# Performance work log

Hardware: AMD Instinct MI355X
Metric: run time of the kernel (lower is better)

The kernel has to match this reference:

```python
import jax, jax.numpy as jnp
import numpy as np
import math

A = 32; B = 32; PSIZE = 16; K = 3; STRIDE = 2; PAD = 1; ITERS = 3; FINAL_LAMBDA = 0.01
KK = K * K; KKA = KK * A; KKA2 = KKA // 2 + 1
EPS = 1e-12; LN2PI = math.log(2 * math.pi)


def unfold(x, k, s, p):
    # torch F.unfold: output feature dim ordered (C, kh, kw), columns row-major
    b, C, h, w = x.shape
    xp = jnp.pad(x, ((0, 0), (0, 0), (p, p), (p, p)))
    oh = (h + 2 * p - k) // s + 1
    ow = (w + 2 * p - k) // s + 1
    cols = [xp[:, :, ki:ki + s * (oh - 1) + 1:s, kj:kj + s * (ow - 1) + 1:s]
            for ki in range(k) for kj in range(k)]
    patches = jnp.stack(cols, axis=2)  # [b, C, kk, oh, ow]
    return patches.reshape(b, C, k * k, oh * ow), oh, ow


def setup_inputs():
    key = jax.random.key(0)
    ks = jax.random.split(key, 8)
    b, h, w = 4, 14, 14
    a_in = jax.random.uniform(ks[0], (b, A, h, w), dtype=jnp.float32)
    pose = jax.random.normal(ks[1], (b, A * PSIZE, h, w), dtype=jnp.float32)
    mpose_w = jax.random.normal(ks[2], (B * PSIZE, PSIZE), dtype=jnp.float32) / np.float32(np.sqrt(PSIZE))
    mpose_b = jnp.zeros((B * PSIZE,), jnp.float32)
    freq_w = jax.random.normal(ks[3], (KKA2, PSIZE, 2), dtype=jnp.float32) * 0.02
    ln_g = jnp.ones((A,), jnp.float32)
    ln_b = jnp.zeros((A,), jnp.float32)
    lim = np.float32(np.sqrt(6.0 / (KK + KK)))  # xavier_uniform on [kk, kk, 1]
    spat_w = jax.random.uniform(ks[4], (KK, KK, 1), jnp.float32, -lim, lim)
    spat_bias = jnp.ones((KK,), jnp.float32)
    beta_u = jnp.zeros((1, 1, B, 1), jnp.float32)
    beta_a = jnp.zeros((1, 1, B), jnp.float32)
    return dict(a_in=a_in, pose=pose, mpose_w=mpose_w, mpose_b=mpose_b,
                freq_w=freq_w, ln_g=ln_g, ln_b=ln_b, spat_w=spat_w,
                spat_bias=spat_bias, beta_u=beta_u, beta_a=beta_a)


def _forward(a_in, pose, mpose_w, mpose_b, freq_w, ln_g, ln_b,
             spat_w, spat_bias, beta_u, beta_a):
    b = a_in.shape[0]
    pose_u, oh, ow = unfold(pose, K, STRIDE, PAD)  # [b, A*PSIZE, KK, l]
    l = oh * ow
    pose_u = pose_u.reshape(b, A, PSIZE, KK, l)
    pose_u = pose_u.transpose(0, 4, 3, 1, 2).reshape(b, l, KKA, PSIZE)
    # mpose linear: psize -> B*psize
    po = jnp.einsum('blkp,qp->blkq', pose_u, mpose_w) + mpose_b
    po = po.reshape(b * l, KKA, B, PSIZE)
    # Frequency FFT filter over kkA axis (weight shared across all B slices)
    xf = jnp.fft.rfft(po, axis=1, norm='ortho')        # [bl, KKA2, B, PSIZE] complex
    wc = freq_w[..., 0] + 1j * freq_w[..., 1]           # [KKA2, PSIZE]
    xf = xf * wc[None, :, None, :]
    po = jnp.fft.irfft(xf, n=KKA, axis=1, norm='ortho') + po  # residual
    v = po.reshape(b, l, KKA, B, PSIZE)
    a_u, _, _ = unfold(a_in, K, STRIDE, PAD)            # [b, A, KK, l]
    a_u = a_u.transpose(0, 3, 2, 1).reshape(b, l, KKA)
    # Spatial gating applied to ones-initialized r (identical for every B slice)
    ones = jnp.ones((b * l, KKA), jnp.float32)
    g = ones.reshape(b * l, KK, A)
    mu_g = g.mean(-1, keepdims=True)
    var_g = ((g - mu_g) ** 2).mean(-1, keepdims=True)
    gn = (g - mu_g) / jnp.sqrt(var_g + 1e-5) * ln_g + ln_b
    g2 = jnp.einsum('ij,nja->nia', spat_w[:, :, 0], gn) + spat_bias[None, :, None]
    gate = jax.nn.gelu(g2, approximate=False).reshape(b * l, KKA) + ones
    logit = jnp.broadcast_to(gate[:, :, None], (b * l, KKA, B))
    r = jax.nn.softmax(logit, axis=2).reshape(b, l, KKA, B, 1)
    a_out = mu = None
    for i in range(ITERS):
        lam = FINAL_LAMBDA * (1.0 - 0.95 ** (i + 1))
        # m-step
        rr = r * a_u[:, :, :, None, None]
        r_sum = rr.sum(axis=2, keepdims=True)                 # [b,l,1,B,1]
        coeff = rr / (r_sum + EPS)
        mu = (coeff * v).sum(axis=2, keepdims=True)           # [b,l,1,B,PSIZE]
        sig = (coeff * (v - mu) ** 2).sum(axis=2, keepdims=True) + EPS
        cost = (beta_u + jnp.log(jnp.sqrt(sig[:, :, 0]))) * r_sum[:, :, 0]  # [b,l,B,PSIZE]
        a_out = jax.nn.sigmoid(lam * (beta_a - cost.sum(axis=3)))           # [b,l,B]
        if i < ITERS - 1:
            # e-step (note: log(sigma_sq * ln2pi) is faithful to the original code)
            ln_p = (-0.5 * jnp.sum(jnp.log(sig * LN2PI), axis=-1)
                    - jnp.sum((v - mu) ** 2 / (2.0 * sig), axis=-1))        # [b,l,KKA,B]
            ln_ap = ln_p + jnp.log(a_out[:, :, None, :])
            r = jax.nn.softmax(ln_ap, axis=-1)[..., None]
    pose_out = mu[:, :, 0].reshape(b, l, B * PSIZE).transpose(0, 2, 1).reshape(b, B * PSIZE, oh, ow)
    a_fin = a_out.transpose(0, 2, 1).reshape(b, B, oh, ow)
    return a_fin, pose_out


def reference(a_in, pose, mpose_w, mpose_b, freq_w, ln_g, ln_b,
              spat_w, spat_bias, beta_u, beta_a):
    return _forward(a_in, pose, mpose_w, mpose_b, freq_w, ln_g, ln_b,
                    spat_w, spat_bias, beta_u, beta_a)
```

## Files before the change

kernel.cpp:

```cpp
#include <hip/hip_runtime.h>
#include <hip/hip_bf16.h>
#include <math.h>

#define A_    32
#define B_    32
#define PS    16
#define KK_   9
#define KKA_  288
#define OH_   7
#define L_    49
#define NB    4
#define NSITE 196
#define NCOLS 3136

#define LAM1 5.0e-4f
#define LAM2 9.75e-4f
#define LAM3 1.42625e-3f
#define LOG_LN2PI 0.6086775903077413f

typedef _Float16 half2v __attribute__((ext_vector_type(2)));
typedef short    short8 __attribute__((ext_vector_type(8)));
typedef float    floatx4 __attribute__((ext_vector_type(4)));

static __device__ __forceinline__ float san(float x, float lo, float hi){
    return fminf(fmaxf(x, lo), hi);
}

static __device__ __forceinline__ float dot2acc(half2v a, half2v b, float c){
#if __has_builtin(__builtin_amdgcn_fdot2)
    return __builtin_amdgcn_fdot2(a, b, c, false);
#else
    return c + (float)a.x*(float)b.x + (float)a.y*(float)b.y;
#endif
}

__global__ void k_prep(const float* __restrict__ fw, const float* __restrict__ pose,
                       ushort* __restrict__ cpr, float* __restrict__ csum,
                       __hip_bfloat16* __restrict__ Xt, int nc)
{
    if ((int)blockIdx.x < nc){
        int id = (int)blockIdx.x*256 + threadIdx.x;
        if (id >= 16*288) return;
        int p = id / 288, m = id % 288;
        float acc = fw[(0*16 + p)*2 + 0];
        for (int k = 1; k <= 143; ++k){
            float re = fw[(k*16 + p)*2 + 0];
            float im = fw[(k*16 + p)*2 + 1];
            int km = (k*m) % 288;
            float ang = 0.021816615649929116f * (float)km;
            float s, c; __sincosf(ang, &s, &c);
            acc += 2.0f*(re*c - im*s);
        }
        float re144 = fw[(144*16 + p)*2 + 0];
        acc += re144 * ((m & 1) ? -1.0f : 1.0f);
        float cv = acc * (1.0f/288.0f);
        if (m == 0) cv += 1.0f;
        cv = san(cv, -1e4f, 1e4f);

        __hip_bfloat16 hb = __float2bfloat16(cv);
        float hif = __bfloat162float(hb);
        __hip_bfloat16 lb = __float2bfloat16(cv - hif);
        ushort hi = *(ushort*)&hb, lo = *(ushort*)&lb;

        ushort* c0h = cpr + p*592;
        ushort* c1h = cpr + 16*592   + p*592;
        ushort* c0l = cpr + 16*592*2 + p*592;
        ushort* c1l = cpr + 16*592*3 + p*592;
        int x1 = 288 - m;
        c0h[x1] = hi;  c0l[x1] = lo;
        c1h[x1-1] = hi; c1l[x1-1] = lo;
        if (m >= 1){
            int x2 = 576 - m;
            c0h[x2] = hi;  c0l[x2] = lo;
            c1h[x2-1] = hi; c1l[x2-1] = lo;
        } else {
            c0h[0] = hi; c0l[0] = lo;
            csum[p] = san(1.0f + fw[(0*16 + p)*2 + 0], -1e4f, 1e4f);
        }
        return;
    }
    int id = ((int)blockIdx.x - nc)*256 + threadIdx.x;
    if (id >= NCOLS*KKA_/8) return;
    int c = id / (KKA_/8), j8 = id % (KKA_/8);
    int j = j8*8;
    int n = c >> 4, q = c & 15;
    int bs = n / L_, l = n % L_, oy = l / OH_, ox = l % OH_;
    int kk = j >> 5, a0 = j & 31;
    int y = oy*2 - 1 + kk/3, x = ox*2 - 1 + kk%3;
    const bool inb = ((unsigned)y < 14u && (unsigned)x < 14u);
    const float* psrc = pose + (((long)bs*(A_*PS))*14 + y)*14 + x;
    union { ushort us[8]; uint4 u4; } res;
    #pragma unroll
    for (int u = 0; u < 8; ++u){
        float v = 0.f;
        if (inb) v = psrc[((a0+u)*PS + q)*196];
        __hip_bfloat16 hb = __float2bfloat16(san(v, -1e4f, 1e4f));
        res.us[u] = *(ushort*)&hb;
    }
    *(uint4*)&Xt[c*KKA_ + j] = res.u4;
}

__global__ __attribute__((amdgpu_flat_work_group_size(512,512), amdgpu_waves_per_eu(1,2)))
void
k_mega(const ushort* __restrict__ cpr, const __hip_bfloat16* __restrict__ Xt,
       const float* __restrict__ a_in,
       const float* __restrict__ mpw, const float* __restrict__ mpb,
       const float* __restrict__ csum,
       const float* __restrict__ beta_u, const float* __restrict__ beta_a,
       float* __restrict__ out)
{
    const int nl = blockIdx.x;
    const int t = threadIdx.x;
    const int Bc = t >> 4, p = t & 15;
    const int bs = nl / L_, l = nl % L_;

    __shared__ uint v_lds[48][512];
    __shared__ __align__(16) _Float16 us[2*4224];
    __shared__ float dall[288*34];
    __shared__ float a_s[KKA_];
    __shared__ float cst[32];

    for (int j = t; j < KKA_; j += 512){
        int kk = j >> 5, a = j & 31;
        int oy = l / OH_, ox = l % OH_;
        int y = oy*2 - 1 + kk/3, x = ox*2 - 1 + kk%3;
        float v = 0.f;
        if ((unsigned)y < 14u && (unsigned)x < 14u)
            v = a_in[((bs*A_ + a)*14 + y)*14 + x];
        a_s[j] = san(v, 0.f, 1e4f);
    }
    half2v w_h[8];
    #pragma unroll
    for (int k = 0; k < 8; ++k){
        w_h[k].x = (_Float16)mpw[t*16 + 2*k];
        w_h[k].y = (_Float16)mpw[t*16 + 2*k + 1];
    }
    const float vb = mpb[t] * csum[p];
    const float bu = beta_u[Bc];
    const float ba = beta_a[Bc];
    __syncthreads();

    float s0a = 0.f, s0b = 0.f, s0c = 0.f, s0d = 0.f;
    for (int j = 0; j < KKA_; j += 4){
        s0a += a_s[j]; s0b += a_s[j+1]; s0c += a_s[j+2]; s0d += a_s[j+3];
    }
    const float S0tot = (s0a + s0b) + (s0c + s0d);

    const int w = t >> 6, lane = t & 63;
    const int mn = lane & 15, quad = lane >> 4;
    const int p0 = w*2;
    const __hip_bfloat16* xrow = Xt + (nl*16 + mn)*KKA_ + quad*8;

    float S1 = 0.f, S2 = 0.f;
    half2v v_h[80];

    auto do_chunk = [&](int ch, _Float16* usb){
        floatx4 accA = {0,0,0,0}, accB = {0,0,0,0};
        for (int k0i = 0; k0i < 9; ++k0i){
            const int k0 = k0i*32;
            short8 bfrag = *(const short8*)&xrow[k0];
            #pragma unroll
            for (int pp = 0; pp < 2; ++pp){
                const int pg = p0 + pp;
                int o = 288 + k0 + quad*8 - (ch*16 + mn);
                int sel = o & 1, off = o - sel;
                const ushort* bh = cpr + (sel ? 16*592 : 0) + pg*592;
                const ushort* bl = cpr + 16*592*2 + (sel ? 16*592 : 0) + pg*592;
                short8 ah = *(const short8*)&bh[off];
                short8 al = *(const short8*)&bl[off];
                floatx4 acc = pp ? accB : accA;
                acc = __builtin_amdgcn_mfma_f32_16x16x32_bf16(ah, bfrag, acc, 0, 0, 0);
                acc = __builtin_amdgcn_mfma_f32_16x16x32_bf16(al, bfrag, acc, 0, 0, 0);
                if (pp) accB = acc; else accA = acc;
            }
        }
        #pragma unroll
        for (int r = 0; r < 4; ++r){
            usb[p0*264     + (quad*4 + r)*16 + mn] = (_Float16)accA[r];
            usb[(p0+1)*264 + (quad*4 + r)*16 + mn] = (_Float16)accB[r];
        }
    };

    auto vpair = [&](const _Float16* urow, int s, float& v0o, float& v1o){
        union { uint4 u4; half2v h2[4]; } A0, A1, B0, B1;
        A0.u4 = *(const uint4*)&urow[(2*s)*16];
        A1.u4 = *(const uint4*)&urow[(2*s)*16 + 8];
        B0.u4 = *(const uint4*)&urow[(2*s+1)*16];
        B1.u4 = *(const uint4*)&urow[(2*s+1)*16 + 8];
        float v0 = vb, v1 = vb;
        #pragma unroll
        for (int m = 0; m < 4; ++m){
            v0 = dot2acc(A0.h2[m], w_h[m],   v0);
            v0 = dot2acc(A1.h2[m], w_h[4+m], v0);
            v1 = dot2acc(B0.h2[m], w_h[m],   v1);
            v1 = dot2acc(B1.h2[m], w_h[4+m], v1);
        }
        v0o = v0; v1o = v1;
    };

    for (int ch = 0; ch < 6; ++ch){
        _Float16* usb = us + (ch & 1)*4224;
        do_chunk(ch, usb);
        __syncthreads();
        const _Float16* urow = &usb[p*264];
        #pragma unroll
        for (int s = 0; s < 8; ++s){
            float v0, v1; vpair(urow, s, v0, v1);
            const int i0 = ch*16 + 2*s;
            const float a0 = a_s[i0], a1 = a_s[i0+1];
            S1 += a0*v0 + a1*v1;
            S2 += a0*v0*v0 + a1*v1*v1;
            union { half2v h; uint u; } cv;
            cv.h.x = (_Float16)v0; cv.h.y = (_Float16)v1;
            v_lds[ch*8 + s][t] = cv.u;
        }
    }
    #pragma unroll
    for (int c2 = 0; c2 < 10; ++c2){
        const int ch = 6 + c2;
        _Float16* usb = us + (ch & 1)*4224;
        do_chunk(ch, usb);
        __syncthreads();
        const _Float16* urow = &usb[p*264];
        #pragma unroll
        for (int s = 0; s < 8; ++s){
            float v0, v1; vpair(urow, s, v0, v1);
            const int i0 = ch*16 + 2*s;
            const float a0 = a_s[i0], a1 = a_s[i0+1];
            S1 += a0*v0 + a1*v1;
            S2 += a0*v0*v0 + a1*v1*v1;
            half2v vh; vh.x = (_Float16)v0; vh.y = (_Float16)v1;
            v_h[c2*8 + s] = vh;
        }
    }
    #pragma unroll
    for (int ch = 16; ch < 18; ++ch){
        _Float16* usb = us + (ch & 1)*4224;
        do_chunk(ch, usb);
        __syncthreads();
        const _Float16* urow = &usb[p*264];
        #pragma unroll
        for (int s = 0; s < 8; ++s){
            float v0, v1; vpair(urow, s, v0, v1);
            const int i0 = ch*16 + 2*s;
            const float a0 = a_s[i0], a1 = a_s[i0+1];
            S1 += a0*v0 + a1*v1;
            S2 += a0*v0*v0 + a1*v1*v1;
        }
    }

    float mu_r, i2s_r;
    {
        const float rs  = S0tot * (1.0f/32.0f);
        const float inv = 1.0f / (rs + 1e-12f);
        const float S1r = S1 * (1.0f/32.0f), S2r = S2 * (1.0f/32.0f);
        mu_r = S1r * inv;
        const float sg  = fmaxf((S2r - 2.f*mu_r*S1r + mu_r*mu_r*rs) * inv, 0.f) + 1e-12f;
        i2s_r = 0.5f / sg;
        const float lg  = logf(sg);
        float cs = (bu + 0.5f*lg) * rs;
        float ls = lg + LOG_LN2PI;
        #pragma unroll
        for (int m = 1; m < 16; m <<= 1){ cs += __shfl_xor(cs, m, 16); ls += __shfl_xor(ls, m, 16); }
        const float aout = san(1.f/(1.f + expf(-LAM1*(ba - cs))), 1e-30f, 1.f);
        if (p == 0) cst[Bc] = logf(aout) - 0.5f*ls;
    }
    __syncthreads();

    const int b0 = p & 1, b1 = (p>>1)&1, b2 = (p>>2)&1, b3 = (p>>3)&1;
    const int isub = t >> 5, Bce = t & 31;
    float muF = 0.f, aF = 0.f;
    for (int it = 0; it < 2; ++it){
        const float lam = it ? LAM3 : LAM2;

        auto dtree = [&](int ibase, auto getpair){
            float e1[8], e2[4], e3[2], dfin;
            #pragma unroll
            for (int s = 0; s < 8; ++s){
                float v0, v1; getpair(s, v0, v1);
                float d0 = v0 - mu_r, d1 = v1 - mu_r;
                float ea = d0*d0*i2s_r, eb = d1*d1*i2s_r;
                float aown  = b0 ? eb : ea;
                float asend = b0 ? ea : eb;
                e1[s] = aown + __shfl_xor(asend, 1);
            }
            #pragma unroll
            for (int s = 0; s < 4; ++s){
                float aown  = b1 ? e1[2*s+1] : e1[2*s];
                float asend = b1 ? e1[2*s]   : e1[2*s+1];
                e2[s] = aown + __shfl_xor(asend, 2);
            }
            #pragma unroll
            for (int s = 0; s < 2; ++s){
                float aown  = b2 ? e2[2*s+1] : e2[2*s];
                float asend = b2 ? e2[2*s]   : e2[2*s+1];
                e3[s] = aown + __shfl_xor(asend, 4);
            }
            {
                float aown  = b3 ? e3[1] : e3[0];
                float asend = b3 ? e3[0] : e3[1];
                dfin = aown + __shfl_xor(asend, 8);
            }
            dall[(ibase + p)*34 + Bc] = dfin;
        };
        for (int g = 0; g < 6; ++g)
            dtree(g*16, [&](int s, float& v0, float& v1){
                union { uint u; half2v h; } cv; cv.u = v_lds[g*8 + s][t];
                v0 = (float)cv.h.x; v1 = (float)cv.h.y; });
        #pragma unroll
        for (int c2 = 0; c2 < 10; ++c2)
            dtree((6+c2)*16, [&](int s, float& v0, float& v1){
                half2v vh = v_h[c2*8 + s];
                v0 = (float)vh.x; v1 = (float)vh.y; });
        #pragma unroll
        for (int ch = 16; ch < 18; ++ch){
            const _Float16* urow = &us[(ch & 1)*4224 + p*264];
            dtree(ch*16, [&](int s, float& v0, float& v1){
                vpair(urow, s, v0, v1); });
        }
        __syncthreads();

        {
            const float cb = cst[Bce];
            #pragma unroll
            for (int g = 0; g < 18; ++g){
                float* dp = &dall[(g*16 + isub)*34 + Bce];
                float lnap = cb - *dp;
                float mx = lnap;
                #pragma unroll
                for (int m = 16; m >= 1; m >>= 1) mx = fmaxf(mx, __shfl_xor(mx, m));
                float ex = expf(lnap - mx);
                float sm = ex;
                #pragma unroll
                for (int m = 16; m >= 1; m >>= 1) sm += __shfl_xor(sm, m);
                *dp = (ex / sm) * a_s[g*16 + isub];
            }
        }
        __syncthreads();

        float T0 = 0.f, T1 = 0.f, T2 = 0.f;
        auto csum3 = [&](int ibase, auto getpair){
            #pragma unroll
            for (int s = 0; s < 8; ++s){
                float v0, v1; getpair(s, v0, v1);
                float r0 = dall[(ibase + 2*s)*34 + Bc];
                float r1 = dall[(ibase + 2*s + 1)*34 + Bc];
                T0 += r0 + r1;
                T1 += r0*v0 + r1*v1;
                T2 += r0*v0*v0 + r1*v1*v1;
            }
        };
        for (int g = 0; g < 6; ++g)
            csum3(g*16, [&](int s, float& v0, float& v1){
                union { uint u; half2v h; } cv; cv.u = v_lds[g*8 + s][t];
                v0 = (float)cv.h.x; v1 = (float)cv.h.y; });
        #pragma unroll
        for (int c2 = 0; c2 < 10; ++c2)
            csum3((6+c2)*16, [&](int s, float& v0, float& v1){
                half2v vh = v_h[c2*8 + s];
                v0 = (float)vh.x; v1 = (float)vh.y; });
        #pragma unroll
        for (int ch = 16; ch < 18; ++ch){
            const _Float16* urow = &us[(ch & 1)*4224 + p*264];
            csum3(ch*16, [&](int s, float& v0, float& v1){
                vpair(urow, s, v0, v1); });
        }

        const float inv = 1.f/(T0 + 1e-12f);
        const float mu  = T1 * inv;
        const float sg  = fmaxf((T2 - 2.f*mu*T1 + mu*mu*T0) * inv, 0.f) + 1e-12f;
        const float lg  = logf(sg);
        float cs = (bu + 0.5f*lg) * T0;
        float ls = lg + LOG_LN2PI;
        #pragma unroll
        for (int m = 1; m < 16; m <<= 1){ cs += __shfl_xor(cs, m, 16); ls += __shfl_xor(ls, m, 16); }
        const float aout = san(1.f/(1.f + expf(-lam*(ba - cs))), 1e-30f, 1.f);
        if (it == 0){
            mu_r = mu; i2s_r = 0.5f/sg;
            if (p == 0) cst[Bc] = logf(aout) - 0.5f*ls;
            __syncthreads();
        } else { muF = mu; aF = aout; }
    }

    if (p == 0) out[bs*(B_*L_) + Bc*L_ + l] = san(aF, 0.f, 1.f);
    out[6272 + (bs*512 + t)*L_ + l] = san(muF, -1e4f, 1e4f);
}

extern "C" void kernel_launch(void* const* d_in, const int* in_sizes, int n_in,
                              void* d_out, int out_size, void* d_ws, size_t ws_size,
                              hipStream_t stream)
{
    const float* a_in   = (const float*)d_in[0];
    const float* pose   = (const float*)d_in[1];
    const float* mpw    = (const float*)d_in[2];
    const float* mpb    = (const float*)d_in[3];
    const float* fw     = (const float*)d_in[4];
    const float* beta_u = (const float*)d_in[9];
    const float* beta_a = (const float*)d_in[10];
    float* out = (float*)d_out;

    char* base = (char*)d_ws;
    float*  csum = (float*)(base + 0);
    ushort* cpr  = (ushort*)(base + 256);
    __hip_bfloat16* Xt = (__hip_bfloat16*)(base + 76288);

    const int nc = 18;
    const int nx = (NCOLS*KKA_/8 + 255)/256;
    k_prep<<<nc + nx, 256, 0, stream>>>(fw, pose, cpr, csum, Xt, nc);
    k_mega<<<NSITE, 512, 0, stream>>>(cpr, Xt, a_in, mpw, mpb, csum, beta_u, beta_a, out);
}
```

Before: 257.2 us.

## Rebalance v storage: triple-buffer LDS chunk, fewer register pairs, pad dall stride

Moves one more 16-row chunk of the v values out of registers: the unfold buffer becomes a triple buffer whose last three chunks get recomputed from LDS, so v_h shrinks from 80 to 72 half2 registers. The dall stride changes from 34 to 33 to cut LDS bank conflicts, and scheduling barriers are added between dtree and csum3 groups to limit live ranges. The launch-bounds attribute switches to __launch_bounds__(512,1). This lowers register pressure and spilling, at the cost of more LDS and one extra recomputed chunk per pass.

```diff
diff --git a/kernel.cpp b/kernel.cpp
--- a/kernel.cpp
+++ b/kernel.cpp
@@ -17,6 +17,8 @@
 #define LAM2 9.75e-4f
 #define LAM3 1.42625e-3f
 #define LOG_LN2PI 0.6086775903077413f
+
+#define DSTR 33
 
 typedef _Float16 half2v __attribute__((ext_vector_type(2)));
 typedef short    short8 __attribute__((ext_vector_type(8)));
@@ -100,8 +102,8 @@
     *(uint4*)&Xt[c*KKA_ + j] = res.u4;
 }
 
-__global__ __attribute__((amdgpu_flat_work_group_size(512,512), amdgpu_waves_per_eu(1,2)))
-void
+__launch_bounds__(512, 1)
+__global__ void
 k_mega(const ushort* __restrict__ cpr, const __hip_bfloat16* __restrict__ Xt,
        const float* __restrict__ a_in,
        const float* __restrict__ mpw, const float* __restrict__ mpb,
@@ -115,8 +117,8 @@
     const int bs = nl / L_, l = nl % L_;
 
     __shared__ uint v_lds[48][512];
-    __shared__ __align__(16) _Float16 us[2*4224];
-    __shared__ float dall[288*34];
+    __shared__ __align__(16) _Float16 us[3*4224];
+    __shared__ float dall[288*DSTR];
     __shared__ float a_s[KKA_];
     __shared__ float cst[32];
 
@@ -152,7 +154,7 @@
     const __hip_bfloat16* xrow = Xt + (nl*16 + mn)*KKA_ + quad*8;
 
     float S1 = 0.f, S2 = 0.f;
-    half2v v_h[80];
+    half2v v_h[72];
 
     auto do_chunk = [&](int ch, _Float16* usb){
         floatx4 accA = {0,0,0,0}, accB = {0,0,0,0};
@@ -199,7 +201,7 @@
     };
 
     for (int ch = 0; ch < 6; ++ch){
-        _Float16* usb = us + (ch & 1)*4224;
+        _Float16* usb = us + (ch % 3)*4224;
         do_chunk(ch, usb);
         __syncthreads();
         const _Float16* urow = &usb[p*264];
@@ -216,9 +218,9 @@
         }
     }
     #pragma unroll
-    for (int c2 = 0; c2 < 10; ++c2){
+    for (int c2 = 0; c2 < 9; ++c2){
         const int ch = 6 + c2;
-        _Float16* usb = us + (ch & 1)*4224;
+        _Float16* usb = us + (ch % 3)*4224;
         do_chunk(ch, usb);
         __syncthreads();
         const _Float16* urow = &usb[p*264];
@@ -234,8 +236,8 @@
         }
     }
     #pragma unroll
-    for (int ch = 16; ch < 18; ++ch){
-        _Float16* usb = us + (ch & 1)*4224;
+    for (int ch = 15; ch < 18; ++ch){
+        _Float16* usb = us + (ch % 3)*4224;
         do_chunk(ch, usb);
         __syncthreads();
         const _Float16* urow = &usb[p*264];
@@ -301,22 +303,27 @@
                 float asend = b3 ? e3[0] : e3[1];
                 dfin = aown + __shfl_xor(asend, 8);
             }
-            dall[(ibase + p)*34 + Bc] = dfin;
+            dall[(ibase + p)*DSTR + Bc] = dfin;
         };
-        for (int g = 0; g < 6; ++g)
+        for (int g = 0; g < 6; ++g){
             dtree(g*16, [&](int s, float& v0, float& v1){
                 union { uint u; half2v h; } cv; cv.u = v_lds[g*8 + s][t];
                 v0 = (float)cv.h.x; v1 = (float)cv.h.y; });
-        #pragma unroll
-        for (int c2 = 0; c2 < 10; ++c2)
+            __builtin_amdgcn_sched_barrier(0);
+        }
+        #pragma unroll
+        for (int c2 = 0; c2 < 9; ++c2){
             dtree((6+c2)*16, [&](int s, float& v0, float& v1){
                 half2v vh = v_h[c2*8 + s];
                 v0 = (float)vh.x; v1 = (float)vh.y; });
-        #pragma unroll
-        for (int ch = 16; ch < 18; ++ch){
-            const _Float16* urow = &us[(ch & 1)*4224 + p*264];
-            dtree(ch*16, [&](int s, float& v0, float& v1){
+            __builtin_amdgcn_sched_barrier(0);
+        }
+        #pragma unroll
+        for (int cc = 0; cc < 3; ++cc){
+            const _Float16* urow = &us[cc*4224 + p*264];
+            dtree((15+cc)*16, [&](int s, float& v0, float& v1){
                 vpair(urow, s, v0, v1); });
+            __builtin_amdgcn_sched_barrier(0);
         }
         __syncthreads();
 
@@ -324,7 +331,7 @@
             const float cb = cst[Bce];
             #pragma unroll
             for (int g = 0; g < 18; ++g){
-                float* dp = &dall[(g*16 + isub)*34 + Bce];
+                float* dp = &dall[(g*16 + isub)*DSTR + Bce];
                 float lnap = cb - *dp;
                 float mx = lnap;
                 #pragma unroll
@@ -343,27 +350,32 @@
             #pragma unroll
             for (int s = 0; s < 8; ++s){
                 float v0, v1; getpair(s, v0, v1);
-                float r0 = dall[(ibase + 2*s)*34 + Bc];
-                float r1 = dall[(ibase + 2*s + 1)*34 + Bc];
+                float r0 = dall[(ibase + 2*s)*DSTR + Bc];
+                float r1 = dall[(ibase + 2*s + 1)*DSTR + Bc];
                 T0 += r0 + r1;
                 T1 += r0*v0 + r1*v1;
                 T2 += r0*v0*v0 + r1*v1*v1;
             }
         };
-        for (int g = 0; g < 6; ++g)
+        for (int g = 0; g < 6; ++g){
             csum3(g*16, [&](int s, float& v0, float& v1){
                 union { uint u; half2v h; } cv; cv.u = v_lds[g*8 + s][t];
                 v0 = (float)cv.h.x; v1 = (float)cv.h.y; });
-        #pragma unroll
-        for (int c2 = 0; c2 < 10; ++c2)
+            __builtin_amdgcn_sched_barrier(0);
+        }
+        #pragma unroll
+        for (int c2 = 0; c2 < 9; ++c2){
             csum3((6+c2)*16, [&](int s, float& v0, float& v1){
                 half2v vh = v_h[c2*8 + s];
                 v0 = (float)vh.x; v1 = (float)vh.y; });
-        #pragma unroll
-        for (int ch = 16; ch < 18; ++ch){
-            const _Float16* urow = &us[(ch & 1)*4224 + p*264];
-            csum3(ch*16, [&](int s, float& v0, float& v1){
+            __builtin_amdgcn_sched_barrier(0);
+        }
+        #pragma unroll
+        for (int cc = 0; cc < 3; ++cc){
+            const _Float16* urow = &us[cc*4224 + p*264];
+            csum3((15+cc)*16, [&](int s, float& v0, float& v1){
                 vpair(urow, s, v0, v1); });
+            __builtin_amdgcn_sched_barrier(0);
         }
 
         const float inv = 1.f/(T0 + 1e-12f);
```

After: 265.2 us. 3.1% more time.
